# Optimization experiments

Measured on AMD Instinct MI355X. Metric: run time of the kernel, lower is better.

The kernel has to match this reference:

```python
import jax, jax.numpy as jnp
import numpy as np

B, S, D, H, DH = 2, 2048, 1024, 16, 64
ATTN_SCALE = float(np.sqrt(DH))  # use_attn_scale=True -> sqrt(d_head)
IGNORE = -100000.0


def setup_inputs() -> dict:
    key = jax.random.key(0)
    ks = jax.random.split(key, 8)
    init = 0.02
    return {
        "residual": jax.random.normal(ks[0], (B, S, D), dtype=jnp.float32),
        "x": jax.random.normal(ks[1], (B, S, D), dtype=jnp.float32),
        "W_Q": jax.random.normal(ks[2], (H, D, DH), dtype=jnp.float32) * init,
        "W_K": jax.random.normal(ks[3], (H, D, DH), dtype=jnp.float32) * init,
        "W_V": jax.random.normal(ks[4], (H, D, DH), dtype=jnp.float32) * init,
        "W_O": jax.random.normal(ks[5], (H, DH, D), dtype=jnp.float32) * init,
        "b_Q": jnp.zeros((H, DH), dtype=jnp.float32),
        "b_K": jnp.zeros((H, DH), dtype=jnp.float32),
        "b_V": jnp.zeros((H, DH), dtype=jnp.float32),
        "b_O": jnp.zeros((D,), dtype=jnp.float32),
    }


def reference(residual, x, W_Q, W_K, W_V, W_O, b_Q, b_K, b_V, b_O):
    # QKV projections: [b,s,d] x [h,d,e] -> [b,s,h,e]
    q = jnp.einsum("bsd,hde->bshe", x, W_Q) + b_Q
    k = jnp.einsum("bsd,hde->bshe", x, W_K) + b_K
    v = jnp.einsum("bsd,hde->bshe", x, W_V) + b_V
    # Scores: [b,h,q,k]
    attn_scores = jnp.einsum("bqhe,bkhe->bhqk", q, k) / ATTN_SCALE
    causal = jnp.tril(jnp.ones((S, S), dtype=bool))
    attn_scores = jnp.where(causal, attn_scores, IGNORE)
    pattern = jax.nn.softmax(attn_scores, axis=-1)
    # Weighted values: [b,q,h,e]
    z = jnp.einsum("bkhe,bhqk->bqhe", v, pattern)
    out = jnp.einsum("bqhe,hed->bqd", z, W_O) + b_O
    return (residual, out)
```

## Files before the change

### kernel.cpp

```cpp
#include <hip/hip_runtime.h>
#include <hip/hip_bf16.h>

#define BB 2
#define SS 2048
#define DD 1024
#define HH 16
#define DHD 64

typedef __attribute__((ext_vector_type(8))) short short8;
typedef __attribute__((ext_vector_type(4))) float floatx4;
typedef __attribute__((ext_vector_type(16))) float floatx16;
typedef __attribute__((ext_vector_type(4))) unsigned short ushortx4;

static __device__ __forceinline__ unsigned short f2bf(float f) {
    union { __hip_bfloat16 h; unsigned short u; } cv;
    cv.h = __float2bfloat16(f);
    return cv.u;
}

typedef __attribute__((address_space(1))) const unsigned int* gas_t;
typedef __attribute__((address_space(3))) unsigned int* las_t;
static __device__ __forceinline__ void g2l16(const void* g, void* l) {
    __builtin_amdgcn_global_load_lds((gas_t)g, (las_t)l, 16, 0, 0);
}

#define SW(row, c8) ((c8) ^ ((row) & 7))

static __device__ __forceinline__ unsigned cvt_pk_bf16(float lo, float hi) {
    unsigned r;
    asm("v_cvt_pk_bf16_f32 %0, %1, %2" : "=v"(r) : "v"(lo), "v"(hi));
    return r;
}
static __device__ __forceinline__ void pl32_swap(unsigned &a, unsigned &b) {
    asm("v_permlane32_swap_b32 %0, %1" : "+v"(a), "+v"(b));
}

__global__ __launch_bounds__(256) void prep(const float4* __restrict__ residual4,
        float4* __restrict__ out4,
        const float* __restrict__ x, unsigned short* __restrict__ xb,
        const float* __restrict__ WQ, const float* __restrict__ WK,
        const float* __restrict__ WV, unsigned short* __restrict__ Wt,
        const float* __restrict__ WO, unsigned short* __restrict__ WtO) {
    __shared__ float tile[64][65];
    const int bid = blockIdx.x;
    const int t = threadIdx.x;

    if (bid < 1024) {
        size_t base = (size_t)bid * 1024 + t;
#pragma unroll
        for (int j = 0; j < 4; j++) out4[base + j * 256] = residual4[base + j * 256];
    } else if (bid < 3072) {
        size_t i = ((size_t)(bid - 1024) * 256 + t) * 8;
        const float4* src4 = (const float4*)(x + i);
        float4 a = src4[0], b = src4[1];
        short8 o;
        o[0] = (short)f2bf(a.x); o[1] = (short)f2bf(a.y);
        o[2] = (short)f2bf(a.z); o[3] = (short)f2bf(a.w);
        o[4] = (short)f2bf(b.x); o[5] = (short)f2bf(b.y);
        o[6] = (short)f2bf(b.z); o[7] = (short)f2bf(b.w);
        *(short8*)(xb + i) = o;
    } else if (bid < 3840) {
        int u = bid - 3072;
        const int d0 = (u & 15) * 64;
        const int h  = (u >> 4) & 15;
        const int which = u >> 8;
        const float* W = (which == 0) ? WQ : (which == 1) ? WK : WV;
        const float* src = W + (size_t)h * DD * DHD;
#pragma unroll
        for (int i = 0; i < 16; i++) {
            int idx = i * 256 + t;
            int r = idx >> 6, c = idx & 63;
            tile[r][c] = src[(size_t)(d0 + r) * DHD + c];
        }
        __syncthreads();
        unsigned short* dst = Wt + ((size_t)which * 1024 + h * 64) * DD;
#pragma unroll
        for (int i = 0; i < 16; i++) {
            int idx = i * 256 + t;
            int e = idx >> 6, d = idx & 63;
            dst[(size_t)e * DD + d0 + d] = f2bf(tile[d][e]);
        }
    } else {
        int u = bid - 3840;
        const int k0 = (u & 15) * 64;
        const int n0 = (u >> 4) * 64;
#pragma unroll
        for (int i = 0; i < 16; i++) {
            int idx = i * 256 + t;
            int r = idx >> 6, c = idx & 63;
            tile[r][c] = WO[(size_t)(k0 + r) * DD + n0 + c];
        }
        __syncthreads();
#pragma unroll
        for (int i = 0; i < 16; i++) {
            int idx = i * 256 + t;
            int n = idx >> 6, kk = idx & 63;
            WtO[(size_t)(n0 + n) * DD + k0 + kk] = f2bf(tile[kk][n]);
        }
    }
}

__global__ __launch_bounds__(256) void qkv_mfma(const unsigned short* __restrict__ xb,
        const unsigned short* __restrict__ Wt,
        const float* __restrict__ bQ, const float* __restrict__ bK,
        const float* __restrict__ bV,
        unsigned short* __restrict__ oq, unsigned short* __restrict__ ok,
        unsigned short* __restrict__ ov) {
    __shared__ unsigned short smem[32768];

    const int m0 = blockIdx.x * 128;
    const int y  = blockIdx.y;
    const int which = y >> 3;
    const int h0 = (y & 7) * 2;
    const float* bias = (which == 0) ? bQ : (which == 1) ? bK : bV;
    unsigned short* ob = (which == 0) ? oq : (which == 1) ? ok : ov;
    const float scale = (which == 0) ? 0.18033688f : 1.0f;
    const unsigned short* Wb = Wt + (size_t)y * 128 * DD;

    const int t = threadIdx.x;
    const int lane = t & 63, w = t >> 6;
    const int l15 = lane & 15, quad = lane >> 4;

    floatx4 acc[2][8];
#pragma unroll
    for (int mt = 0; mt < 2; mt++)
#pragma unroll
        for (int nt = 0; nt < 8; nt++) acc[mt][nt] = floatx4{0.f, 0.f, 0.f, 0.f};

#pragma unroll
    for (int i = 0; i < 4; i++) {
        int c = i * 256 + t;
        int row = c >> 3, c8 = c & 7;
        g2l16(xb + (size_t)(m0 + row) * DD + SW(row, c8) * 8, smem + c * 8);
        g2l16(Wb + (size_t)row * DD + SW(row, c8) * 8, smem + 16384 + c * 8);
    }

    int buf = 0;
    for (int k0 = 0; k0 < DD; k0 += 64) {
        __syncthreads();
        if (k0 + 64 < DD) {
            const int nb = buf ^ 1;
#pragma unroll
            for (int i = 0; i < 4; i++) {
                int c = i * 256 + t;
                int row = c >> 3, c8 = c & 7;
                g2l16(xb + (size_t)(m0 + row) * DD + k0 + 64 + SW(row, c8) * 8,
                      smem + nb * 8192 + c * 8);
                g2l16(Wb + (size_t)row * DD + k0 + 64 + SW(row, c8) * 8,
                      smem + 16384 + nb * 8192 + c * 8);
            }
        }
        const unsigned short* As = smem + buf * 8192;
        const unsigned short* Bs = smem + 16384 + buf * 8192;
#pragma unroll
        for (int ks = 0; ks < 2; ks++) {
            short8 af[2], bf[8];
#pragma unroll
            for (int mt = 0; mt < 2; mt++)
                af[mt] = *(const short8*)(As + (w * 32 + mt * 16 + l15) * 64 +
                                          SW(l15, ks * 4 + quad) * 8);
#pragma unroll
            for (int nt = 0; nt < 8; nt++)
                bf[nt] = *(const short8*)(Bs + (nt * 16 + l15) * 64 +
                                          SW(l15, ks * 4 + quad) * 8);
#pragma unroll
            for (int mt = 0; mt < 2; mt++)
#pragma unroll
                for (int nt = 0; nt < 8; nt++)
                    acc[mt][nt] = __builtin_amdgcn_mfma_f32_16x16x32_bf16(
                        af[mt], bf[nt], acc[mt][nt], 0, 0, 0);
        }
        buf ^= 1;
    }
    __syncthreads();

    if (which == 2) {
        unsigned short* T = smem;
#pragma unroll
        for (int mt = 0; mt < 2; mt++)
#pragma unroll
            for (int r = 0; r < 4; r++) {
                int mloc = w * 32 + mt * 16 + quad * 4 + r;
#pragma unroll
                for (int nt = 0; nt < 8; nt++) {
                    int n = nt * 16 + l15;
                    int h = h0 + (n >> 6), e = n & 63;
                    T[n * 132 + mloc] = f2bf(acc[mt][nt][r] + bias[h * DHD + e]);
                }
            }
        __syncthreads();
        const int b = m0 >> 11;
        const int s_base = m0 & (SS - 1);
#pragma unroll
        for (int i = 0; i < 8; i++) {
            int u = i * 256 + t;
            int row = u >> 4, c8 = u & 15;
            int h = h0 + (row >> 6), e = row & 63;
            *(short8*)(ov + (((size_t)b * HH + h) * DHD + e) * SS + s_base + c8 * 8) =
                *(const short8*)(T + row * 132 + c8 * 8);
        }
    } else {
#pragma unroll
        for (int mt = 0; mt < 2; mt++) {
#pragma unroll
            for (int r = 0; r < 4; r++) {
                int m = m0 + w * 32 + mt * 16 + quad * 4 + r;
                int b = m >> 11, s = m & (SS - 1);
#pragma unroll
                for (int nt = 0; nt < 8; nt++) {
                    int h = h0 + (nt >> 2);
                    int e = (nt & 3) * 16 + l15;
                    float v = (acc[mt][nt][r] + bias[h * DHD + e]) * scale;
                    ob[(((size_t)b * HH + h) * SS + s) * DHD + e] = f2bf(v);
                }
            }
        }
    }
}

#define KVT 128
__global__ __launch_bounds__(512, 4) void attn(const unsigned short* __restrict__ q,
        const unsigned short* __restrict__ k, const unsigned short* __restrict__ vt,
        unsigned short* __restrict__ z) {
    __shared__ unsigned short smem[32768];

    const int i0 = blockIdx.x;
    int bh, qt;
    if (i0 < 256) { bh = i0 & 31;         qt = 15 - (i0 >> 5); }
    else          { bh = (i0 - 256) & 31; qt = (i0 - 256) >> 5; }
    const int b  = bh >> 4, h = bh & (HH - 1);
    const int q0 = qt * 128;

    const int t = threadIdx.x;
    const int lane = t & 63;
    const int w = t >> 6;
    const int qsub = w & 3;
    const int grp  = w >> 2;
    const int l31 = lane & 31;
    const int hi = lane >> 5;

    const unsigned short* qb  = q  + (size_t)bh * SS * DHD;
    const unsigned short* kb  = k  + (size_t)bh * SS * DHD;
    const unsigned short* vtb = vt + (size_t)bh * DHD * SS;

    const int qrow = q0 + qsub * 32 + l31;
    const int fmin = q0 + qsub * 32;

    short8 qf[4];
#pragma unroll
    for (int c = 0; c < 4; c++)
        qf[c] = *(const short8*)(qb + (size_t)qrow * DHD + c * 16 + hi * 8);

    floatx16 o_acc[2];
#pragma unroll
    for (int eh = 0; eh < 2; eh++)
#pragma unroll
        for (int i = 0; i < 16; i++) o_acc[eh][i] = 0.f;
    float lsum = 0.f;

    int koff[4], voff[4];
#pragma unroll
    for (int c = 0; c < 4; c++)
        koff[c] = (grp * 64 + l31) * 64 + (((2 * c + hi) ^ (l31 & 7)) * 8);
#pragma unroll
    for (int ch = 0; ch < 4; ch++)
        voff[ch] = l31 * 128 + (((grp * 8 + ch * 2 + hi) ^ (l31 & 15)) * 8);

    const int nit = qt + 1;

#pragma unroll
    for (int i = 0; i < 2; i++) {
        int u = i * 512 + t, r = u >> 3, c8 = u & 7;
        g2l16(kb + (size_t)r * DHD + (c8 ^ (r & 7)) * 8, smem + u * 8);
    }
#pragma unroll
    for (int i = 0; i < 2; i++) {
        int u = i * 512 + t, e = u >> 4, c16 = u & 15;
        g2l16(vtb + (size_t)e * SS + (c16 ^ (e & 15)) * 8, smem + 16384 + u * 8);
    }

    for (int it = 0; it < nit; it++) {
        const int cur = it & 1;
        __syncthreads();
        if (it + 1 < nit) {
            const int nxt = cur ^ 1;
            const int kbase = (it + 1) * KVT;
#pragma unroll
            for (int i = 0; i < 2; i++) {
                int u = i * 512 + t, r = u >> 3, c8 = u & 7;
                g2l16(kb + (size_t)(kbase + r) * DHD + (c8 ^ (r & 7)) * 8,
                      smem + nxt * 8192 + u * 8);
            }
#pragma unroll
            for (int i = 0; i < 2; i++) {
                int u = i * 512 + t, e = u >> 4, c16 = u & 15;
                g2l16(vtb + (size_t)e * SS + kbase + (c16 ^ (e & 15)) * 8,
                      smem + 16384 + nxt * 8192 + u * 8);
            }
        }

        const unsigned short* Kc = smem + cur * 8192;
        const unsigned short* Vc = smem + 16384 + cur * 8192;
        const int tb = it * KVT + grp * 64;
        const bool alive0 = (tb      <= fmin + 31);
        const bool alive1 = (tb + 32 <= fmin + 31);

        short8 pb[4];

#pragma unroll
        for (int st = 0; st < 2; st++) {
            const bool alive = st ? alive1 : alive0;
            if (!alive) continue;
            const int kvb = tb + st * 32;

            floatx16 sacc;
#pragma unroll
            for (int i = 0; i < 16; i++) sacc[i] = 0.f;
            __builtin_amdgcn_s_setprio(1);
#pragma unroll
            for (int c = 0; c < 4; c++) {
                short8 af = *(const short8*)(Kc + st * 2048 + koff[c]);
                sacc = __builtin_amdgcn_mfma_f32_32x32x16_bf16(af, qf[c], sacc,
                                                               0, 0, 0);
            }
            __builtin_amdgcn_s_setprio(0);

            unsigned wv[8];
            if (kvb + 31 <= fmin) {
#pragma unroll
                for (int r2 = 0; r2 < 8; r2++) {
                    float p0 = __builtin_amdgcn_exp2f(sacc[2 * r2]);
                    float p1 = __builtin_amdgcn_exp2f(sacc[2 * r2 + 1]);
                    lsum += p0 + p1;
                    wv[r2] = cvt_pk_bf16(p0, p1);
                }
            } else {
#pragma unroll
                for (int r2 = 0; r2 < 8; r2++) {
                    const int ra = 2 * r2, rb = 2 * r2 + 1;
                    const int kva = kvb + (ra & 3) + 8 * (ra >> 2) + 4 * hi;
                    const int kvc = kvb + (rb & 3) + 8 * (rb >> 2) + 4 * hi;
                    float p0 = (kva <= qrow) ? __builtin_amdgcn_exp2f(sacc[ra]) : 0.f;
                    float p1 = (kvc <= qrow) ? __builtin_amdgcn_exp2f(sacc[rb]) : 0.f;
                    lsum += p0 + p1;
                    wv[r2] = cvt_pk_bf16(p0, p1);
                }
            }
            pl32_swap(wv[0], wv[2]);
            pl32_swap(wv[1], wv[3]);
            pl32_swap(wv[4], wv[6]);
            pl32_swap(wv[5], wv[7]);
            union { unsigned u[4]; short8 s; } u0, u1;
            u0.u[0] = wv[0]; u0.u[1] = wv[1]; u0.u[2] = wv[2]; u0.u[3] = wv[3];
            u1.u[0] = wv[4]; u1.u[1] = wv[5]; u1.u[2] = wv[6]; u1.u[3] = wv[7];
            pb[2 * st]     = u0.s;
            pb[2 * st + 1] = u1.s;
        }

        __builtin_amdgcn_s_setprio(1);
#pragma unroll
        for (int ch = 0; ch < 4; ch++) {
            if (!((ch >> 1) ? alive1 : alive0)) continue;
#pragma unroll
            for (int eh = 0; eh < 2; eh++) {
                short8 vf = *(const short8*)(Vc + eh * 4096 + voff[ch]);
                o_acc[eh] = __builtin_amdgcn_mfma_f32_32x32x16_bf16(
                    vf, pb[ch], o_acc[eh], 0, 0, 0);
            }
        }
        __builtin_amdgcn_s_setprio(0);
    }

    lsum += __shfl_xor(lsum, 32);
    float* cm = (float*)smem;
    float* slot = cm + (qsub * 64 + lane) * 33;
    __syncthreads();
    if (grp == 1) {
#pragma unroll
        for (int eh = 0; eh < 2; eh++)
#pragma unroll
            for (int i = 0; i < 16; i++) slot[eh * 16 + i] = o_acc[eh][i];
        slot[32] = lsum;
    }
    __syncthreads();
    if (grp == 0) {
#pragma unroll
        for (int eh = 0; eh < 2; eh++)
#pragma unroll
            for (int i = 0; i < 16; i++) o_acc[eh][i] += slot[eh * 16 + i];
        const float inv = 1.f / (lsum + slot[32]);
        unsigned short* zr = z + ((size_t)b * SS + qrow) * (HH * DHD) + h * DHD;
#pragma unroll
        for (int eh = 0; eh < 2; eh++)
#pragma unroll
            for (int g = 0; g < 4; g++) {
                ushortx4 o;
#pragma unroll
                for (int m = 0; m < 4; m++) o[m] = f2bf(o_acc[eh][g * 4 + m] * inv);
                *(ushortx4*)(zr + eh * 32 + g * 8 + 4 * hi) = o;
            }
    }
}

__global__ __launch_bounds__(256) void out_mfma(const unsigned short* __restrict__ zb,
        const unsigned short* __restrict__ WtO, const float* __restrict__ bo,
        float* __restrict__ out) {
    __shared__ unsigned short smem[24576];

    const int m0 = blockIdx.x * 128;
    const int n0 = blockIdx.y * 64;
    const int t = threadIdx.x;
    const int lane = t & 63, w = t >> 6;
    const int l15 = lane & 15, quad = lane >> 4;

    floatx4 acc[2][4];
#pragma unroll
    for (int mt = 0; mt < 2; mt++)
#pragma unroll
        for (int nt = 0; nt < 4; nt++) acc[mt][nt] = floatx4{0.f, 0.f, 0.f, 0.f};

#pragma unroll
    for (int i = 0; i < 4; i++) {
        int c = i * 256 + t;
        int row = c >> 3, c8 = c & 7;
        g2l16(zb + (size_t)(m0 + row) * DD + SW(row, c8) * 8, smem + c * 8);
    }
#pragma unroll
    for (int i = 0; i < 2; i++) {
        int c = i * 256 + t;
        int row = c >> 3, c8 = c & 7;
        g2l16(WtO + (size_t)(n0 + row) * DD + SW(row, c8) * 8, smem + 16384 + c * 8);
    }

    int buf = 0;
    for (int k0 = 0; k0 < DD; k0 += 64) {
        __syncthreads();
        if (k0 + 64 < DD) {
            const int nb = buf ^ 1;
#pragma unroll
            for (int i = 0; i < 4; i++) {
                int c = i * 256 + t;
                int row = c >> 3, c8 = c & 7;
                g2l16(zb + (size_t)(m0 + row) * DD + k0 + 64 + SW(row, c8) * 8,
                      smem + nb * 8192 + c * 8);
            }
#pragma unroll
            for (int i = 0; i < 2; i++) {
                int c = i * 256 + t;
                int row = c >> 3, c8 = c & 7;
                g2l16(WtO + (size_t)(n0 + row) * DD + k0 + 64 + SW(row, c8) * 8,
                      smem + 16384 + nb * 4096 + c * 8);
            }
        }
        const unsigned short* As = smem + buf * 8192;
        const unsigned short* Bs = smem + 16384 + buf * 4096;
#pragma unroll
        for (int ks = 0; ks < 2; ks++) {
            short8 af[2], bf[4];
#pragma unroll
            for (int mt = 0; mt < 2; mt++)
                af[mt] = *(const short8*)(As + (w * 32 + mt * 16 + l15) * 64 +
                                          SW(l15, ks * 4 + quad) * 8);
#pragma unroll
            for (int nt = 0; nt < 4; nt++)
                bf[nt] = *(const short8*)(Bs + (nt * 16 + l15) * 64 +
                                          SW(l15, ks * 4 + quad) * 8);
#pragma unroll
            for (int mt = 0; mt < 2; mt++)
#pragma unroll
                for (int nt = 0; nt < 4; nt++)
                    acc[mt][nt] = __builtin_amdgcn_mfma_f32_16x16x32_bf16(
                        af[mt], bf[nt], acc[mt][nt], 0, 0, 0);
        }
        buf ^= 1;
    }
#pragma unroll
    for (int mt = 0; mt < 2; mt++) {
#pragma unroll
        for (int r = 0; r < 4; r++) {
            int m = m0 + w * 32 + mt * 16 + quad * 4 + r;
#pragma unroll
            for (int nt = 0; nt < 4; nt++) {
                int n = n0 + nt * 16 + l15;
                out[(size_t)m * DD + n] = acc[mt][nt][r] + bo[n];
            }
        }
    }
}

extern "C" void kernel_launch(void* const* d_in, const int* in_sizes, int n_in,
                              void* d_out, int out_size, void* d_ws, size_t ws_size,
                              hipStream_t stream) {
    const float* residual = (const float*)d_in[0];
    const float* x   = (const float*)d_in[1];
    const float* W_Q = (const float*)d_in[2];
    const float* W_K = (const float*)d_in[3];
    const float* W_V = (const float*)d_in[4];
    const float* W_O = (const float*)d_in[5];
    const float* b_Q = (const float*)d_in[6];
    const float* b_K = (const float*)d_in[7];
    const float* b_V = (const float*)d_in[8];
    const float* b_O = (const float*)d_in[9];
    float* out = (float*)d_out;

    const size_t NE = (size_t)BB * SS * HH * DHD;
    unsigned short* xb  = (unsigned short*)d_ws;
    unsigned short* Wt  = xb + (size_t)4096 * 1024;
    unsigned short* WtO = Wt + (size_t)3072 * 1024;
    unsigned short* qb  = WtO + (size_t)1024 * 1024;
    unsigned short* kb  = qb + NE;
    unsigned short* vb  = kb + NE;
    unsigned short* zb  = vb + NE;

    prep<<<4096, 256, 0, stream>>>((const float4*)residual, (float4*)out,
                                   x, xb, W_Q, W_K, W_V, Wt, W_O, WtO);

    qkv_mfma<<<dim3(32, 24), 256, 0, stream>>>(xb, Wt, b_Q, b_K, b_V, qb, kb, vb);

    attn<<<512, 512, 0, stream>>>(qb, kb, vb, zb);

    out_mfma<<<dim3(32, 16), 256, 0, stream>>>(
        zb, WtO, b_O, out + (size_t)BB * SS * DD);
}
```

Baseline: 179.9 us.

## Load K and V fragments directly from global memory instead of LDS staging

Removes the double-buffered LDS staging of K and V tiles in the attention kernel. Each wave now reads its MFMA operands straight from global memory with per-lane pointers that advance by one KV tile per iteration. This drops the per-iteration barrier and the shrinks shared memory to the final reduction buffer, which may raise occupancy. In exchange, K and V are re-read by every wave group, relying on cache hits, and global-load latency is exposed directly in the MFMA loop without explicit prefetch.

```diff
diff --git a/kernel.cpp b/kernel.cpp
--- a/kernel.cpp
+++ b/kernel.cpp
@@ -222,7 +222,7 @@
 __global__ __launch_bounds__(512, 4) void attn(const unsigned short* __restrict__ q,
         const unsigned short* __restrict__ k, const unsigned short* __restrict__ vt,
         unsigned short* __restrict__ z) {
-    __shared__ unsigned short smem[32768];
+    __shared__ float cm[8448];
 
     const int i0 = blockIdx.x;
     int bh, qt;
@@ -258,49 +258,14 @@
         for (int i = 0; i < 16; i++) o_acc[eh][i] = 0.f;
     float lsum = 0.f;
 
-    int koff[4], voff[4];
-#pragma unroll
-    for (int c = 0; c < 4; c++)
-        koff[c] = (grp * 64 + l31) * 64 + (((2 * c + hi) ^ (l31 & 7)) * 8);
-#pragma unroll
-    for (int ch = 0; ch < 4; ch++)
-        voff[ch] = l31 * 128 + (((grp * 8 + ch * 2 + hi) ^ (l31 & 15)) * 8);
+    const unsigned short* ka0 = kb + (size_t)(grp * 64 + l31) * DHD + hi * 8;
+    const unsigned short* ka1 = ka0 + 32 * DHD;
+    const unsigned short* va0 = vtb + (size_t)l31 * SS + grp * 64 + hi * 8;
+    const unsigned short* va1 = va0 + (size_t)32 * SS;
 
     const int nit = qt + 1;
 
-#pragma unroll
-    for (int i = 0; i < 2; i++) {
-        int u = i * 512 + t, r = u >> 3, c8 = u & 7;
-        g2l16(kb + (size_t)r * DHD + (c8 ^ (r & 7)) * 8, smem + u * 8);
-    }
-#pragma unroll
-    for (int i = 0; i < 2; i++) {
-        int u = i * 512 + t, e = u >> 4, c16 = u & 15;
-        g2l16(vtb + (size_t)e * SS + (c16 ^ (e & 15)) * 8, smem + 16384 + u * 8);
-    }
-
     for (int it = 0; it < nit; it++) {
-        const int cur = it & 1;
-        __syncthreads();
-        if (it + 1 < nit) {
-            const int nxt = cur ^ 1;
-            const int kbase = (it + 1) * KVT;
-#pragma unroll
-            for (int i = 0; i < 2; i++) {
-                int u = i * 512 + t, r = u >> 3, c8 = u & 7;
-                g2l16(kb + (size_t)(kbase + r) * DHD + (c8 ^ (r & 7)) * 8,
-                      smem + nxt * 8192 + u * 8);
-            }
-#pragma unroll
-            for (int i = 0; i < 2; i++) {
-                int u = i * 512 + t, e = u >> 4, c16 = u & 15;
-                g2l16(vtb + (size_t)e * SS + kbase + (c16 ^ (e & 15)) * 8,
-                      smem + 16384 + nxt * 8192 + u * 8);
-            }
-        }
-
-        const unsigned short* Kc = smem + cur * 8192;
-        const unsigned short* Vc = smem + 16384 + cur * 8192;
         const int tb = it * KVT + grp * 64;
         const bool alive0 = (tb      <= fmin + 31);
         const bool alive1 = (tb + 32 <= fmin + 31);
@@ -312,6 +277,7 @@
             const bool alive = st ? alive1 : alive0;
             if (!alive) continue;
             const int kvb = tb + st * 32;
+            const unsigned short* ap = st ? ka1 : ka0;
 
             floatx16 sacc;
 #pragma unroll
@@ -319,7 +285,7 @@
             __builtin_amdgcn_s_setprio(1);
 #pragma unroll
             for (int c = 0; c < 4; c++) {
-                short8 af = *(const short8*)(Kc + st * 2048 + koff[c]);
+                short8 af = *(const short8*)(ap + c * 16);
                 sacc = __builtin_amdgcn_mfma_f32_32x32x16_bf16(af, qf[c], sacc,
                                                                0, 0, 0);
             }
@@ -361,20 +327,21 @@
 #pragma unroll
         for (int ch = 0; ch < 4; ch++) {
             if (!((ch >> 1) ? alive1 : alive0)) continue;
-#pragma unroll
-            for (int eh = 0; eh < 2; eh++) {
-                short8 vf = *(const short8*)(Vc + eh * 4096 + voff[ch]);
-                o_acc[eh] = __builtin_amdgcn_mfma_f32_32x32x16_bf16(
-                    vf, pb[ch], o_acc[eh], 0, 0, 0);
-            }
+            short8 vf0 = *(const short8*)(va0 + ch * 16);
+            o_acc[0] = __builtin_amdgcn_mfma_f32_32x32x16_bf16(
+                vf0, pb[ch], o_acc[0], 0, 0, 0);
+            short8 vf1 = *(const short8*)(va1 + ch * 16);
+            o_acc[1] = __builtin_amdgcn_mfma_f32_32x32x16_bf16(
+                vf1, pb[ch], o_acc[1], 0, 0, 0);
         }
         __builtin_amdgcn_s_setprio(0);
+
+        ka0 += KVT * DHD; ka1 += KVT * DHD;
+        va0 += KVT;       va1 += KVT;
     }
 
     lsum += __shfl_xor(lsum, 32);
-    float* cm = (float*)smem;
     float* slot = cm + (qsub * 64 + lane) * 33;
-    __syncthreads();
     if (grp == 1) {
 #pragma unroll
         for (int eh = 0; eh < 2; eh++)
```

Result: slower. 219.1 us (+21.7%).
